# Optimization experiments

Hardware: AMD Instinct MI355X
Metric: run time of the kernel (lower is better)

## Reference

```python
import jax, jax.numpy as jnp
import numpy as np

B, T, D = 4, 2048, 2048
NUM_HEADS = 16
NUM_KV_HEADS = 4
HEAD_DIM = D // NUM_HEADS  # 128
KV_GROUPS = NUM_HEADS // NUM_KV_HEADS  # 4
ROPE_THETA = 10000.0


def _rope_tables(seq_len, head_dim, theta):
    inv_freq = 1.0 / theta ** (jnp.arange(0, head_dim, 2, dtype=jnp.float32) / head_dim)
    t = jnp.arange(seq_len, dtype=jnp.float32)
    freqs = jnp.outer(t, inv_freq)  # (T, head_dim//2)
    return jnp.cos(freqs), jnp.sin(freqs)


def _apply_rotary(x, cos, sin):
    # x: (B, H, T, d); cos/sin: (T, d//2)
    d = x.shape[-1]
    x1, x2 = x[..., : d // 2], x[..., d // 2:]
    c = cos[None, None, :, :]
    s = sin[None, None, :, :]
    return jnp.concatenate([x1 * c - x2 * s, x1 * s + x2 * c], axis=-1)


def setup_inputs() -> dict:
    key = jax.random.key(0)
    kx, kq, kk, kv, ko = jax.random.split(key, 5)
    scale = 1.0 / np.sqrt(D)
    return {
        "x": jax.random.normal(kx, (B, T, D), dtype=jnp.float32),
        "Wq": jax.random.normal(kq, (NUM_HEADS * HEAD_DIM, D), dtype=jnp.float32) * scale,
        "Wk": jax.random.normal(kk, (NUM_KV_HEADS * HEAD_DIM, D), dtype=jnp.float32) * scale,
        "Wv": jax.random.normal(kv, (NUM_KV_HEADS * HEAD_DIM, D), dtype=jnp.float32) * scale,
        "Wo": jax.random.normal(ko, (D, D), dtype=jnp.float32) * scale,
    }


def reference(x, Wq, Wk, Wv, Wo):
    Bc, Tc, Dc = x.shape
    # projections (Linear with weight (out,in): y = x @ W.T)
    q = (x @ Wq.T).reshape(Bc, Tc, NUM_HEADS, HEAD_DIM).transpose(0, 2, 1, 3)
    k = (x @ Wk.T).reshape(Bc, Tc, NUM_KV_HEADS, HEAD_DIM).transpose(0, 2, 1, 3)
    v = (x @ Wv.T).reshape(Bc, Tc, NUM_KV_HEADS, HEAD_DIM).transpose(0, 2, 1, 3)

    cos, sin = _rope_tables(Tc, HEAD_DIM, ROPE_THETA)
    q = _apply_rotary(q, cos, sin)
    k = _apply_rotary(k, cos, sin)

    # grouped-query attention: broadcast KV heads instead of repeat_interleave
    # q: (B, kvH, G, T, d); k,v: (B, kvH, T, d)
    qg = q.reshape(Bc, NUM_KV_HEADS, KV_GROUPS, Tc, HEAD_DIM)
    scores = jnp.einsum("bkgtd,bksd->bkgts", qg, k) / jnp.sqrt(jnp.float32(HEAD_DIM))
    causal = jnp.tril(jnp.ones((Tc, Tc), dtype=bool))
    scores = jnp.where(causal[None, None, None], scores, jnp.float32(-jnp.inf))
    attn = jax.nn.softmax(scores, axis=-1)
    out = jnp.einsum("bkgts,bksd->bkgtd", attn, v)  # (B, kvH, G, T, d)
    out = out.reshape(Bc, NUM_HEADS, Tc, HEAD_DIM).transpose(0, 2, 1, 3).reshape(Bc, Tc, Dc)
    return out @ Wo.T
```

## Files before the change

kernel.cpp:

```cpp
#include <hip/hip_runtime.h>
#include <stdint.h>

#define B_ 4
#define T_ 2048
#define D_ 2048
#define NH_ 16
#define NKV_ 4
#define HD_ 128
#define QKVN 3072
#define QSCALE_ 0.1275174334161689f

typedef unsigned short u16;
typedef __attribute__((ext_vector_type(8))) short short8;
typedef __attribute__((ext_vector_type(4))) float floatx4;

typedef __attribute__((address_space(1))) void* gas_p;
typedef __attribute__((address_space(3))) void* las_p;

__device__ __forceinline__ u16 f2bf(float f) {
  union { float f; uint32_t u; } a; a.f = f;
  uint32_t r = a.u + 0x7fffu + ((a.u >> 16) & 1u);
  return (u16)(r >> 16);
}
__device__ __forceinline__ float bf2f(u16 u) {
  union { uint32_t u; float f; } a; a.u = ((uint32_t)u) << 16;
  return a.f;
}
__device__ __forceinline__ void gl_lds16(const u16* g, u16* l) {
  __builtin_amdgcn_global_load_lds((gas_p)g, (las_p)l, 16, 0, 0);
}

__global__ void cvt_kernel(const float* __restrict__ in, u16* __restrict__ out, int n) {
  int i = blockIdx.x * 256 + threadIdx.x;
  if (i * 4 >= n) return;
  float4 v = ((const float4*)in)[i];
  union { u16 u[4]; uint2 v2; } o;
  o.u[0] = f2bf(v.x); o.u[1] = f2bf(v.y); o.u[2] = f2bf(v.z); o.u[3] = f2bf(v.w);
  ((uint2*)out)[i] = o.v2;
}

__global__ void rope_tables_kernel(float* __restrict__ tabs) {
  int i = blockIdx.x * 256 + threadIdx.x;
  if (i >= T_ * 64) return;
  int t = i >> 6, d = i & 63;
  float inv = powf(10000.0f, -(float)d / 64.0f);
  float f = (float)t * inv;
  tabs[i] = cosf(f);
  tabs[T_ * 64 + i] = sinf(f);
}

__global__ void rope_q_kernel(const u16* __restrict__ qkv, const float* __restrict__ tabs,
                              u16* __restrict__ q_r) {
  int i = blockIdx.x * 256 + threadIdx.x;
  if (i >= B_ * T_ * NH_ * 64) return;
  int d = i & 63;
  int h = (i >> 6) & 15;
  int t = (i >> 10) & 2047;
  int b = i >> 21;
  size_t row = (size_t)(b * T_ + t) * QKVN + h * HD_;
  float x1 = bf2f(qkv[row + d]);
  float x2 = bf2f(qkv[row + d + 64]);
  float c = tabs[t * 64 + d];
  float s = tabs[T_ * 64 + t * 64 + d];
  size_t ob = ((size_t)(b * NH_ + h) * T_ + t) * HD_;
  q_r[ob + d] = f2bf((x1 * c - x2 * s) * QSCALE_);
  q_r[ob + d + 64] = f2bf((x1 * s + x2 * c) * QSCALE_);
}

__global__ void rope_k_kernel(const u16* __restrict__ qkv, const float* __restrict__ tabs,
                              u16* __restrict__ k_r) {
  int i = blockIdx.x * 256 + threadIdx.x;
  if (i >= B_ * T_ * NKV_ * 64) return;
  int d = i & 63;
  int kh = (i >> 6) & 3;
  int t = (i >> 8) & 2047;
  int b = i >> 19;
  size_t row = (size_t)(b * T_ + t) * QKVN + D_ + kh * HD_;
  float x1 = bf2f(qkv[row + d]);
  float x2 = bf2f(qkv[row + d + 64]);
  float c = tabs[t * 64 + d];
  float s = tabs[T_ * 64 + t * 64 + d];
  size_t ob = ((size_t)(b * NKV_ + kh) * T_ + t) * HD_;
  k_r[ob + d] = f2bf(x1 * c - x2 * s);
  k_r[ob + d + 64] = f2bf(x1 * s + x2 * c);
}

__global__ void v_trans_kernel(const u16* __restrict__ qkv, u16* __restrict__ v_t) {
  __shared__ u16 tile[64 * 128];
  int bk = blockIdx.y;
  int b = bk >> 2, kh = bk & 3;
  int t0 = blockIdx.x * 64;
#pragma unroll
  for (int rep = 0; rep < 32; rep++) {
    int idx = rep * 256 + threadIdx.x;
    int tt = idx >> 7, d = idx & 127;
    tile[idx] = qkv[(size_t)(b * T_ + t0 + tt) * QKVN + D_ + 512 + kh * HD_ + d];
  }
  __syncthreads();
#pragma unroll
  for (int rep = 0; rep < 32; rep++) {
    int idx = rep * 256 + threadIdx.x;
    int d = idx >> 6, tt = idx & 63;
    v_t[((size_t)bk * HD_ + d) * T_ + t0 + tt] = tile[tt * 128 + d];
  }
}

template <int OUTF32>
__global__ __launch_bounds__(512, 2)
void gemm_bt256(const u16* __restrict__ A, const u16* __restrict__ Bm,
                void* __restrict__ Cv, int M, int N, int K) {
  __shared__ u16 As[2][256 * 64];
  __shared__ u16 Bs[2][256 * 64];
  const int tid = threadIdx.x;
  const int wave = tid >> 6, lane = tid & 63;
  const int l16 = lane & 15, quad = lane >> 4;

  const int gx = gridDim.x;
  const int nwg = gx * gridDim.y;
  const int orig = blockIdx.y * gx + blockIdx.x;
  const int cpx = nwg >> 3;
  const int swid = (orig & 7) * cpx + (orig >> 3);
  const int m0 = (swid / gx) * 256, n0 = (swid % gx) * 256;
  const int wm = (wave >> 2) * 128, wn = (wave & 3) * 64;

  floatx4 acc[8][4];
#pragma unroll
  for (int i = 0; i < 8; i++)
#pragma unroll
    for (int j = 0; j < 4; j++)
#pragma unroll
      for (int r = 0; r < 4; r++) acc[i][j][r] = 0.0f;

  const u16* gA[4]; const u16* gB[4];
  u16* lA0[4]; u16* lA1[4]; u16* lB0[4]; u16* lB1[4];
#pragma unroll
  for (int rep = 0; rep < 4; rep++) {
    int u = rep * 512 + tid;
    int row = u >> 3;
    int ks = (u & 7) ^ (row & 7);
    gA[rep] = A + (size_t)(m0 + row) * K + ks * 8;
    gB[rep] = Bm + (size_t)(n0 + row) * K + ks * 8;
    lA0[rep] = &As[0][u * 8]; lA1[rep] = &As[1][u * 8];
    lB0[rep] = &Bs[0][u * 8]; lB1[rep] = &Bs[1][u * 8];
  }

#pragma unroll
  for (int rep = 0; rep < 4; rep++) {
    gl_lds16(gA[rep], lA0[rep]);
    gl_lds16(gB[rep], lB0[rep]);
  }

  const int NT = K >> 6;
#pragma unroll 1
  for (int kt = 0; kt < NT; kt++) {
    const int cur = kt & 1;
    __syncthreads();
    if (kt + 1 < NT) {
#pragma unroll
      for (int rep = 0; rep < 4; rep++) {
        gl_lds16(gA[rep] + 64, cur ? lA0[rep] : lA1[rep]);
        gl_lds16(gB[rep] + 64, cur ? lB0[rep] : lB1[rep]);
        gA[rep] += 64; gB[rep] += 64;
      }
      __builtin_amdgcn_sched_barrier(0);
    }
    const u16* ab = &As[cur][0];
    const u16* bb = &Bs[cur][0];
#pragma unroll
    for (int kc = 0; kc < 2; kc++) {
      const int kq = (kc * 4 + quad) ^ (l16 & 7);
      short8 af[8], bfv[4];
#pragma unroll
      for (int i = 0; i < 8; i++)
        af[i] = *(const short8*)(ab + ((wm + i * 16 + l16) * 8 + kq) * 8);
#pragma unroll
      for (int j = 0; j < 4; j++)
        bfv[j] = *(const short8*)(bb + ((wn + j * 16 + l16) * 8 + kq) * 8);
      __builtin_amdgcn_s_setprio(1);
#pragma unroll
      for (int i = 0; i < 8; i++)
#pragma unroll
        for (int j = 0; j < 4; j++)
          acc[i][j] = __builtin_amdgcn_mfma_f32_16x16x32_bf16(af[i], bfv[j], acc[i][j], 0, 0, 0);
      __builtin_amdgcn_s_setprio(0);
    }
  }

#pragma unroll
  for (int i = 0; i < 8; i++)
#pragma unroll
    for (int j = 0; j < 4; j++)
#pragma unroll
      for (int r = 0; r < 4; r++) {
        int m = m0 + wm + i * 16 + quad * 4 + r;
        int n = n0 + wn + j * 16 + l16;
        if (OUTF32)
          ((float*)Cv)[(size_t)m * N + n] = acc[i][j][r];
        else
          ((u16*)Cv)[(size_t)m * N + n] = f2bf(acc[i][j][r]);
      }
}

__global__ __launch_bounds__(256)
void attn_fused(const u16* __restrict__ q_r, const u16* __restrict__ k_r,
                const u16* __restrict__ v_t, u16* __restrict__ outp) {
  __shared__ u16 Ks[64 * 128];
  __shared__ u16 Vs[64 * 128];
  __shared__ u16 Ps[4][32 * 64];
  const int tid = threadIdx.x;
  const int wave = tid >> 6, lane = tid & 63;
  const int l16 = lane & 15, quad = lane >> 4;
  const int bh = blockIdx.y;
  const int b = bh >> 4, h = bh & 15;
  const int kh = h >> 2;

  const u16* qhead = q_r + (size_t)bh * T_ * HD_;
  const u16* khead = k_r + (size_t)(b * NKV_ + kh) * T_ * HD_;
  const u16* vhead = v_t + (size_t)(b * NKV_ + kh) * HD_ * T_;

  int uu[4], kv_j[4], kv_kb[4], v_jo[4], v_k2[4], nn16[4], qq[4];
#pragma unroll
  for (int rep = 0; rep < 4; rep++) {
    int u = rep * 256 + tid;
    uu[rep] = u;
    nn16[rep] = u & 15; qq[rep] = (u >> 4) & 3;
    kv_j[rep] = (u >> 6) & 3; kv_kb[rep] = (u >> 8) & 3;
    v_jo[rep] = (u >> 6) & 7; v_k2[rep] = (u >> 9) & 1;
  }

  const short8 ones = { 0x3F80, 0x3F80, 0x3F80, 0x3F80, 0x3F80, 0x3F80, 0x3F80, 0x3F80 };
  char* psb = (char*)&Ps[wave][0];
  const int swz = (l16 & 7) << 4;

  for (int pass = 0; pass < 2; pass++) {
    const int qtile = pass ? (15 - (int)blockIdx.x) : (int)blockIdx.x;
    const int qbase = qtile * 128;
    const int ntiles = 2 * qtile + 2;

    short8 qf[2][4];
#pragma unroll
    for (int i = 0; i < 2; i++) {
      int t = qbase + wave * 32 + i * 16 + l16;
#pragma unroll
      for (int kb = 0; kb < 4; kb++)
        qf[i][kb] = *(const short8*)(qhead + (size_t)t * HD_ + kb * 32 + quad * 8);
    }

    const u16* kg[4]; const u16* vg[4]; u16* kl[4]; u16* vl[4];
#pragma unroll
    for (int rep = 0; rep < 4; rep++) {
      kg[rep] = khead + (size_t)(kv_j[rep] * 16 + nn16[rep]) * HD_ + kv_kb[rep] * 32 + qq[rep] * 8;
      vg[rep] = vhead + (size_t)(v_jo[rep] * 16 + nn16[rep]) * T_ + v_k2[rep] * 32 + qq[rep] * 8;
      kl[rep] = &Ks[uu[rep] * 8];
      vl[rep] = &Vs[uu[rep] * 8];
    }

    floatx4 acc_o[2][8];
    floatx4 acc_l[2];
#pragma unroll
    for (int i = 0; i < 2; i++) {
#pragma unroll
      for (int jo = 0; jo < 8; jo++)
#pragma unroll
        for (int r = 0; r < 4; r++) acc_o[i][jo][r] = 0.0f;
#pragma unroll
      for (int r = 0; r < 4; r++) acc_l[i][r] = 0.0f;
    }

    for (int tile = 0; tile < ntiles; tile++) {
      const int kv0 = tile * 64;
#pragma unroll
      for (int rep = 0; rep < 4; rep++) {
        gl_lds16(kg[rep], kl[rep]);
        gl_lds16(vg[rep], vl[rep]);
        kg[rep] += 64 * HD_;
        vg[rep] += 64;
      }
      __syncthreads();

      floatx4 s_acc[2][4];
#pragma unroll
      for (int i = 0; i < 2; i++)
#pragma unroll
        for (int j = 0; j < 4; j++)
#pragma unroll
          for (int r = 0; r < 4; r++) s_acc[i][j][r] = 0.0f;
      __builtin_amdgcn_s_setprio(1);
#pragma unroll
      for (int kb = 0; kb < 4; kb++) {
        short8 bk[4];
#pragma unroll
        for (int j = 0; j < 4; j++)
          bk[j] = *(const short8*)(Ks + (((kb * 4 + j) * 4 + quad) * 16 + l16) * 8);
#pragma unroll
        for (int i = 0; i < 2; i++)
#pragma unroll
          for (int j = 0; j < 4; j++)
            s_acc[i][j] = __builtin_amdgcn_mfma_f32_16x16x32_bf16(bk[j], qf[i][kb], s_acc[i][j], 0, 0, 0);
      }
      __builtin_amdgcn_s_setprio(0);

      if (tile + 2 >= ntiles) {
#pragma unroll
        for (int i = 0; i < 2; i++) {
          const int qg = qbase + wave * 32 + i * 16 + l16;
          const int prow = i * 16 + l16;
#pragma unroll
          for (int j = 0; j < 4; j++) {
            const int kg0 = kv0 + j * 16 + quad * 4;
            float p0 = (kg0 + 0 > qg) ? 0.0f : exp2f(s_acc[i][j][0]);
            float p1 = (kg0 + 1 > qg) ? 0.0f : exp2f(s_acc[i][j][1]);
            float p2 = (kg0 + 2 > qg) ? 0.0f : exp2f(s_acc[i][j][2]);
            float p3 = (kg0 + 3 > qg) ? 0.0f : exp2f(s_acc[i][j][3]);
            uint32_t lo, hi;
            asm("v_cvt_pk_bf16_f32 %0, %1, %2" : "=v"(lo) : "v"(p0), "v"(p1));
            asm("v_cvt_pk_bf16_f32 %0, %1, %2" : "=v"(hi) : "v"(p2), "v"(p3));
            uint2 pk; pk.x = lo; pk.y = hi;
            *(uint2*)(psb + ((prow * 128 + j * 32 + quad * 8) ^ swz)) = pk;
          }
        }
      } else {
#pragma unroll
        for (int i = 0; i < 2; i++) {
          const int prow = i * 16 + l16;
#pragma unroll
          for (int j = 0; j < 4; j++) {
            float p0 = exp2f(s_acc[i][j][0]);
            float p1 = exp2f(s_acc[i][j][1]);
            float p2 = exp2f(s_acc[i][j][2]);
            float p3 = exp2f(s_acc[i][j][3]);
            uint32_t lo, hi;
            asm("v_cvt_pk_bf16_f32 %0, %1, %2" : "=v"(lo) : "v"(p0), "v"(p1));
            asm("v_cvt_pk_bf16_f32 %0, %1, %2" : "=v"(hi) : "v"(p2), "v"(p3));
            uint2 pk; pk.x = lo; pk.y = hi;
            *(uint2*)(psb + ((prow * 128 + j * 32 + quad * 8) ^ swz)) = pk;
          }
        }
      }

      __builtin_amdgcn_s_setprio(1);
#pragma unroll
      for (int k2 = 0; k2 < 2; k2++) {
        short8 ap[2];
#pragma unroll
        for (int i = 0; i < 2; i++) {
          const int prow = i * 16 + l16;
          ap[i] = *(const short8*)(psb + ((prow * 128 + k2 * 64 + quad * 16) ^ swz));
        }
#pragma unroll
        for (int jo = 0; jo < 8; jo++) {
          short8 bv = *(const short8*)(Vs + (((k2 * 8 + jo) * 4 + quad) * 16 + l16) * 8);
          acc_o[0][jo] = __builtin_amdgcn_mfma_f32_16x16x32_bf16(ap[0], bv, acc_o[0][jo], 0, 0, 0);
          acc_o[1][jo] = __builtin_amdgcn_mfma_f32_16x16x32_bf16(ap[1], bv, acc_o[1][jo], 0, 0, 0);
        }
        acc_l[0] = __builtin_amdgcn_mfma_f32_16x16x32_bf16(ap[0], ones, acc_l[0], 0, 0, 0);
        acc_l[1] = __builtin_amdgcn_mfma_f32_16x16x32_bf16(ap[1], ones, acc_l[1], 0, 0, 0);
      }
      __builtin_amdgcn_s_setprio(0);
      __syncthreads();
    }

#pragma unroll
    for (int i = 0; i < 2; i++)
#pragma unroll
      for (int r = 0; r < 4; r++) {
        const float inv = 1.0f / acc_l[i][r];
        const int t = qbase + wave * 32 + i * 16 + quad * 4 + r;
        u16* orow = outp + ((size_t)(b * T_ + t)) * D_ + h * HD_;
#pragma unroll
        for (int jo = 0; jo < 8; jo++)
          orow[jo * 16 + l16] = f2bf(acc_o[i][jo][r] * inv);
      }
    __syncthreads();
  }
}

extern "C" void kernel_launch(void* const* d_in, const int* in_sizes, int n_in,
                              void* d_out, int out_size, void* d_ws, size_t ws_size,
                              hipStream_t stream) {
  const float* x  = (const float*)d_in[0];
  const float* Wq = (const float*)d_in[1];
  const float* Wk = (const float*)d_in[2];
  const float* Wv = (const float*)d_in[3];
  const float* Wo = (const float*)d_in[4];

  char* ws = (char*)d_ws;
  u16* xbf  = (u16*)(ws);
  u16* attn = xbf;
  u16* qkv  = (u16*)(ws + 33554432);
  u16* wcat = (u16*)(ws + 83886080);
  u16* wobf = (u16*)(ws + 96468992);
  u16* qr   = (u16*)(ws + 104857600);
  u16* kr   = (u16*)(ws + 138412032);
  u16* vt   = (u16*)(ws + 146800640);
  float* tabs = (float*)(ws + 155189248);

  cvt_kernel<<<16384, 256, 0, stream>>>(x, xbf, 16777216);
  cvt_kernel<<<4096, 256, 0, stream>>>(Wq, wcat, 4194304);
  cvt_kernel<<<1024, 256, 0, stream>>>(Wk, wcat + 4194304, 1048576);
  cvt_kernel<<<1024, 256, 0, stream>>>(Wv, wcat + 5242880, 1048576);
  cvt_kernel<<<4096, 256, 0, stream>>>(Wo, wobf, 4194304);
  rope_tables_kernel<<<512, 256, 0, stream>>>(tabs);

  gemm_bt256<0><<<dim3(12, 32), 512, 0, stream>>>(xbf, wcat, (void*)qkv, 8192, 3072, 2048);

  rope_q_kernel<<<32768, 256, 0, stream>>>(qkv, tabs, qr);
  rope_k_kernel<<<8192, 256, 0, stream>>>(qkv, tabs, kr);
  v_trans_kernel<<<dim3(32, 16), 256, 0, stream>>>(qkv, vt);

  attn_fused<<<dim3(8, 64), 256, 0, stream>>>(qr, kr, vt, attn);

  gemm_bt256<1><<<dim3(8, 32), 512, 0, stream>>>(attn, wobf, d_out, 8192, 2048, 2048);
}
```

Before: 460.8 us.

## Double-buffer K/V tiles in attention with 512-thread blocks and XCD-aware mapping

The attention kernel moves to 8-wave blocks that each cover 256 query rows per pass, so every K/V tile loaded into LDS serves twice as many queries. K/V tiles are now double-buffered: the next tile's global-to-LDS load is issued before computing on the current tile, which also removes one barrier per iteration. Block indices are remapped so blocks sharing a KV head land on the same XCD, aiming for better L2 reuse. The cost is double the LDS per block, possibly lower occupancy, and coarser work units for causal load balancing.

Result: no change. 454.6 us (-1.4%).

```diff
diff --git a/kernel.cpp b/kernel.cpp
--- a/kernel.cpp
+++ b/kernel.cpp
@@ -201,27 +201,33 @@
       }
 }
 
-__global__ __launch_bounds__(256)
+__global__ __launch_bounds__(512, 2)
 void attn_fused(const u16* __restrict__ q_r, const u16* __restrict__ k_r,
                 const u16* __restrict__ v_t, u16* __restrict__ outp) {
-  __shared__ u16 Ks[64 * 128];
-  __shared__ u16 Vs[64 * 128];
-  __shared__ u16 Ps[4][32 * 64];
+  __shared__ u16 Ks[2][64 * 128];
+  __shared__ u16 Vs[2][64 * 128];
+  __shared__ u16 Ps[8][32 * 64];
   const int tid = threadIdx.x;
   const int wave = tid >> 6, lane = tid & 63;
   const int l16 = lane & 15, quad = lane >> 4;
-  const int bh = blockIdx.y;
-  const int b = bh >> 4, h = bh & 15;
-  const int kh = h >> 2;
+
+  const int L = (int)blockIdx.y * 4 + (int)blockIdx.x;
+  const int xcd = L & 7, slot = L >> 3;
+  const int grp = (xcd << 1) | (slot >> 4);
+  const int j16 = slot & 15;
+  const int b = grp >> 2, kh = grp & 3;
+  const int h = (kh << 2) | (j16 >> 2);
+  const int qpair = j16 & 3;
+  const int bh = b * NH_ + h;
 
   const u16* qhead = q_r + (size_t)bh * T_ * HD_;
   const u16* khead = k_r + (size_t)(b * NKV_ + kh) * T_ * HD_;
   const u16* vhead = v_t + (size_t)(b * NKV_ + kh) * HD_ * T_;
 
-  int uu[4], kv_j[4], kv_kb[4], v_jo[4], v_k2[4], nn16[4], qq[4];
-#pragma unroll
-  for (int rep = 0; rep < 4; rep++) {
-    int u = rep * 256 + tid;
+  int uu[2], kv_j[2], kv_kb[2], v_jo[2], v_k2[2], nn16[2], qq[2];
+#pragma unroll
+  for (int rep = 0; rep < 2; rep++) {
+    int u = rep * 512 + tid;
     uu[rep] = u;
     nn16[rep] = u & 15; qq[rep] = (u >> 4) & 3;
     kv_j[rep] = (u >> 6) & 3; kv_kb[rep] = (u >> 8) & 3;
@@ -233,9 +239,9 @@
   const int swz = (l16 & 7) << 4;
 
   for (int pass = 0; pass < 2; pass++) {
-    const int qtile = pass ? (15 - (int)blockIdx.x) : (int)blockIdx.x;
-    const int qbase = qtile * 128;
-    const int ntiles = 2 * qtile + 2;
+    const int qtile = pass ? (7 - qpair) : qpair;
+    const int qbase = qtile * 256;
+    const int ntiles = 4 * qtile + 4;
 
     short8 qf[2][4];
 #pragma unroll
@@ -246,13 +252,14 @@
         qf[i][kb] = *(const short8*)(qhead + (size_t)t * HD_ + kb * 32 + quad * 8);
     }
 
-    const u16* kg[4]; const u16* vg[4]; u16* kl[4]; u16* vl[4];
-#pragma unroll
-    for (int rep = 0; rep < 4; rep++) {
+    const u16* kg[2]; const u16* vg[2];
+    u16* klb[2][2]; u16* vlb[2][2];
+#pragma unroll
+    for (int rep = 0; rep < 2; rep++) {
       kg[rep] = khead + (size_t)(kv_j[rep] * 16 + nn16[rep]) * HD_ + kv_kb[rep] * 32 + qq[rep] * 8;
       vg[rep] = vhead + (size_t)(v_jo[rep] * 16 + nn16[rep]) * T_ + v_k2[rep] * 32 + qq[rep] * 8;
-      kl[rep] = &Ks[uu[rep] * 8];
-      vl[rep] = &Vs[uu[rep] * 8];
+      klb[rep][0] = &Ks[0][uu[rep] * 8]; klb[rep][1] = &Ks[1][uu[rep] * 8];
+      vlb[rep][0] = &Vs[0][uu[rep] * 8]; vlb[rep][1] = &Vs[1][uu[rep] * 8];
     }
 
     floatx4 acc_o[2][8];
@@ -267,16 +274,31 @@
       for (int r = 0; r < 4; r++) acc_l[i][r] = 0.0f;
     }
 
+#pragma unroll
+    for (int rep = 0; rep < 2; rep++) {
+      gl_lds16(kg[rep], klb[rep][0]);
+      gl_lds16(vg[rep], vlb[rep][0]);
+      kg[rep] += 64 * HD_;
+      vg[rep] += 64;
+    }
+
+#pragma unroll 1
     for (int tile = 0; tile < ntiles; tile++) {
       const int kv0 = tile * 64;
-#pragma unroll
-      for (int rep = 0; rep < 4; rep++) {
-        gl_lds16(kg[rep], kl[rep]);
-        gl_lds16(vg[rep], vl[rep]);
-        kg[rep] += 64 * HD_;
-        vg[rep] += 64;
-      }
+      const int cur = tile & 1;
       __syncthreads();
+      if (tile + 1 < ntiles) {
+#pragma unroll
+        for (int rep = 0; rep < 2; rep++) {
+          gl_lds16(kg[rep], klb[rep][cur ^ 1]);
+          gl_lds16(vg[rep], vlb[rep][cur ^ 1]);
+          kg[rep] += 64 * HD_;
+          vg[rep] += 64;
+        }
+        __builtin_amdgcn_sched_barrier(0);
+      }
+      const u16* ksb = &Ks[cur][0];
+      const u16* vsb = &Vs[cur][0];
 
       floatx4 s_acc[2][4];
 #pragma unroll
@@ -291,7 +313,7 @@
         short8 bk[4];
 #pragma unroll
         for (int j = 0; j < 4; j++)
-          bk[j] = *(const short8*)(Ks + (((kb * 4 + j) * 4 + quad) * 16 + l16) * 8);
+          bk[j] = *(const short8*)(ksb + (((kb * 4 + j) * 4 + quad) * 16 + l16) * 8);
 #pragma unroll
         for (int i = 0; i < 2; i++)
 #pragma unroll
@@ -300,7 +322,7 @@
       }
       __builtin_amdgcn_s_setprio(0);
 
-      if (tile + 2 >= ntiles) {
+      if (tile + 4 >= ntiles) {
 #pragma unroll
         for (int i = 0; i < 2; i++) {
           const int qg = qbase + wave * 32 + i * 16 + l16;
@@ -349,7 +371,7 @@
         }
 #pragma unroll
         for (int jo = 0; jo < 8; jo++) {
-          short8 bv = *(const short8*)(Vs + (((k2 * 8 + jo) * 4 + quad) * 16 + l16) * 8);
+          short8 bv = *(const short8*)(vsb + (((k2 * 8 + jo) * 4 + quad) * 16 + l16) * 8);
           acc_o[0][jo] = __builtin_amdgcn_mfma_f32_16x16x32_bf16(ap[0], bv, acc_o[0][jo], 0, 0, 0);
           acc_o[1][jo] = __builtin_amdgcn_mfma_f32_16x16x32_bf16(ap[1], bv, acc_o[1][jo], 0, 0, 0);
         }
@@ -357,7 +379,6 @@
         acc_l[1] = __builtin_amdgcn_mfma_f32_16x16x32_bf16(ap[1], ones, acc_l[1], 0, 0, 0);
       }
       __builtin_amdgcn_s_setprio(0);
-      __syncthreads();
     }
 
 #pragma unroll
@@ -408,7 +429,7 @@
   rope_k_kernel<<<8192, 256, 0, stream>>>(qkv, tabs, kr);
   v_trans_kernel<<<dim3(32, 16), 256, 0, stream>>>(qkv, vt);
 
-  attn_fused<<<dim3(8, 64), 256, 0, stream>>>(qr, kr, vt, attn);
+  attn_fused<<<dim3(4, 64), 512, 0, stream>>>(qr, kr, vt, attn);
 
   gemm_bt256<1><<<dim3(8, 32), 512, 0, stream>>>(attn, wobf, d_out, 8192, 2048, 2048);
 }
```
